# Kernel tuning notes

Hardware: AMD Instinct MI355X
Metric: run time of the kernel (lower is better)

## Reference

```python
import jax, jax.numpy as jnp
import numpy as np

N, E, D = 50000, 800000, 128   # nodes, edges, input feature dim
HEADS, HC = 8, 16
H = HEADS * HC                 # 128 hidden width after concat
G, OUT = 64, 16                # graphs in batch, output classes
EPS_BN = 1e-5


def _gat_conv(x, src, dst, edge_attr, W, att_src, att_dst, We, att_edge, b):
    """PyG GATConv (concat=True, negative_slope=0.2, add_self_loops=True,
    fill_value='mean' for edge_attr, dropout inactive in eval)."""
    n = x.shape[0]
    # self-loop edge attr = per-node mean of incoming edge attrs
    ones = jnp.ones((src.shape[0], 1), x.dtype)
    deg = jax.ops.segment_sum(ones, dst, num_segments=n)
    ea_mean = jax.ops.segment_sum(edge_attr, dst, num_segments=n) / jnp.maximum(deg, 1.0)
    loop = jnp.arange(n, dtype=src.dtype)
    src_f = jnp.concatenate([src, loop])
    dst_f = jnp.concatenate([dst, loop])
    ea = jnp.concatenate([edge_attr, ea_mean])          # [E+N, 1]
    h = (x @ W).reshape(n, HEADS, HC)                   # [N, heads, hc]
    a_src = jnp.sum(h * att_src, axis=-1)               # [N, heads]
    a_dst = jnp.sum(h * att_dst, axis=-1)               # [N, heads]
    he = (ea @ We).reshape(-1, HEADS, HC)               # [E+N, heads, hc]
    a_e = jnp.sum(he * att_edge, axis=-1)               # [E+N, heads]
    alpha = jax.nn.leaky_relu(a_src[src_f] + a_dst[dst_f] + a_e, 0.2)
    # segment softmax over destination nodes
    amax = jax.ops.segment_max(alpha, dst_f, num_segments=n)
    ex = jnp.exp(alpha - amax[dst_f])
    denom = jax.ops.segment_sum(ex, dst_f, num_segments=n)
    coef = ex / (denom[dst_f] + 1e-16)                  # [E+N, heads]
    out = jax.ops.segment_sum(h[src_f] * coef[..., None], dst_f, num_segments=n)
    return out.reshape(n, H) + b


def setup_inputs() -> dict:
    key = jax.random.key(0)
    k = lambda i: jax.random.fold_in(key, i)
    nrm = lambda i, shape, s=0.1: jax.random.normal(k(i), shape, dtype=jnp.float32) * s
    inp = {
        "x": jax.random.normal(k(0), (N, D), dtype=jnp.float32),
        "edge_index": jax.random.randint(k(1), (2, E), 0, N, dtype=jnp.int32),
        "edge_weights": jax.random.normal(k(2), (E, 1), dtype=jnp.float32),
        "batch": jnp.sort(jax.random.randint(k(3), (N,), 0, G, dtype=jnp.int32)),
        "bn_gamma": jnp.ones((D,), jnp.float32),
        "bn_beta": jnp.zeros((D,), jnp.float32),
        "bn_mean": nrm(4, (D,)),
        "bn_var": jax.random.uniform(k(5), (D,), dtype=jnp.float32) + 0.5,
    }
    ci = 10
    for li, ind in [(1, D), (2, H), (3, H)]:
        inp[f"W{li}"] = nrm(ci, (ind, H)); ci += 1
        inp[f"att_src{li}"] = nrm(ci, (HEADS, HC)); ci += 1
        inp[f"att_dst{li}"] = nrm(ci, (HEADS, HC)); ci += 1
        inp[f"We{li}"] = nrm(ci, (1, H)); ci += 1
        inp[f"att_edge{li}"] = nrm(ci, (HEADS, HC)); ci += 1
        inp[f"b{li}"] = jnp.zeros((H,), jnp.float32)
    inp["Wl1"] = nrm(40, (H, 2 * HC)); inp["bl1"] = jnp.zeros((2 * HC,), jnp.float32)
    inp["Wl2"] = nrm(41, (2 * HC, OUT)); inp["bl2"] = jnp.zeros((OUT,), jnp.float32)
    return inp


def reference(x, edge_index, edge_weights, batch,
              bn_gamma, bn_beta, bn_mean, bn_var,
              W1, att_src1, att_dst1, We1, att_edge1, b1,
              W2, att_src2, att_dst2, We2, att_edge2, b2,
              W3, att_src3, att_dst3, We3, att_edge3, b3,
              Wl1, bl1, Wl2, bl2):
    src, dst = edge_index[0], edge_index[1]
    # BatchNorm (eval mode, running stats)
    h = (x - bn_mean) / jnp.sqrt(bn_var + EPS_BN) * bn_gamma + bn_beta
    h = jax.nn.relu(_gat_conv(h, src, dst, edge_weights, W1, att_src1, att_dst1, We1, att_edge1, b1))
    h = jax.nn.relu(_gat_conv(h, src, dst, edge_weights, W2, att_src2, att_dst2, We2, att_edge2, b2))
    h = _gat_conv(h, src, dst, edge_weights, W3, att_src3, att_dst3, We3, att_edge3, b3)
    g = jax.ops.segment_max(h, batch, num_segments=G)   # global max pool -> [G, H]
    g = jax.nn.relu(g @ Wl1 + bl1)
    # dropout p=0.5 is identity in eval mode
    return g @ Wl2 + bl2
```

## Files before the change

kernel.cpp:

```cpp
#include <hip/hip_runtime.h>
#include <math.h>

#define NN 50000
#define NE 800000
#define NH 8
#define HDIM 128
#define NG 64
#define PSPLIT 16
#define MAXD 64

typedef __attribute__((ext_vector_type(8))) short bf16x8;
typedef __attribute__((ext_vector_type(4))) float f32x4;

static __device__ __forceinline__ float lrelu02(float x){ return x > 0.f ? x : 0.2f*x; }
static __device__ __forceinline__ unsigned short f2bf(float f){
    unsigned u = __float_as_uint(f);
    unsigned r = (u + 0x7FFFu + ((u >> 16) & 1u)) >> 16;
    return (unsigned short)r;
}
static __device__ __forceinline__ float bf2f(unsigned short h){ return __uint_as_float((unsigned)h << 16); }
static __device__ __forceinline__ float bf_lo(unsigned v){ return __uint_as_float(v << 16); }
static __device__ __forceinline__ float bf_hi(unsigned v){ return __uint_as_float(v & 0xFFFF0000u); }

__global__ void k_prep(const float* We1, const float* ae1, const float* We2, const float* ae2,
                       const float* We3, const float* ae3, float* wev,
                       const float* gam, const float* bet, const float* mean, const float* var,
                       float* sc, float* sh){
    int t = threadIdx.x;
    if (t < 128){
        float s = gam[t] * rsqrtf(var[t] + 1e-5f);
        sc[t] = s; sh[t] = bet[t] - mean[t] * s;
    } else if (t < 152){
        int q = t - 128; int l = q >> 3, hd = q & 7;
        const float* We = (l == 0) ? We1 : (l == 1) ? We2 : We3;
        const float* ae = (l == 0) ? ae1 : (l == 1) ? ae2 : ae3;
        float s = 0.f;
        for (int c = 0; c < 16; c++) s += We[hd*16+c] * ae[hd*16+c];
        wev[q] = s;
    }
}

__global__ void k_wprep(const float* W1, const float* W2, const float* W3,
                        unsigned short* Wth, unsigned short* Wtl){
    int i = blockIdx.x*256 + threadIdx.x;
    if (i >= 3*16384) return;
    int l = i >> 14, rem = i & 16383;
    int k = rem >> 7, n = rem & 127;
    const float* W = (l==0) ? W1 : (l==1) ? W2 : W3;
    float w = W[k*128 + n];
    unsigned short hi = f2bf(w);
    unsigned short lo = f2bf(w - bf2f(hi));
    Wth[l*16384 + n*128 + k] = hi;
    Wtl[l*16384 + n*128 + k] = lo;
}

__global__ void k_scatter(const int* srcp, const int* dstp, const float* ew,
                          unsigned long long* pk, unsigned* slab){
    int i = blockIdx.x*256 + threadIdx.x;
    if (i >= NE) return;
    int d = dstp[i];
    float w = ew[i];
    int fx = __float2int_rn(w * 16384.f);
    unsigned long long enc = ((unsigned long long)(unsigned)fx << 32) | 1ull;
    unsigned long long old = atomicAdd(&pk[d], enc);
    unsigned rank = (unsigned)(old & 0xFFFFFFFFull);
    if (rank < MAXD){
        unsigned ent = (unsigned)srcp[i] | ((unsigned)f2bf(w) << 16);
        __builtin_nontemporal_store(ent, &slab[(size_t)d*MAXD + rank]);
    }
}

__global__ __launch_bounds__(256, 3) void k_gemm(const float* A,
        const unsigned short* Wth, const unsigned short* Wtl,
        const float* sc, const float* sh,
        const float* att_s, const float* att_d,
        unsigned* Hb, float* a_src, float* a_dst, int M){
    __shared__ unsigned short Ah[64][132];
    __shared__ unsigned short Al[64][132];
    int t = threadIdx.x;
    int row0 = blockIdx.x * 64;
    int w = t >> 6, l = t & 63;
    int lr = l & 15, lg = l >> 4;

    {
        bool bn = (sc != nullptr);
        const float2* A2 = (const float2*)A;
        for (int i = 0; i < 16; i++){
            int idx2 = t + i*256;
            int r = idx2 >> 6, c2 = idx2 & 63;
            float2 v = make_float2(0.f, 0.f);
            if (row0 + r < M){
                v = A2[(size_t)(row0+r)*64 + c2];
                if (bn){
                    float2 s2 = ((const float2*)sc)[c2], h2 = ((const float2*)sh)[c2];
                    v.x = v.x*s2.x + h2.x; v.y = v.y*s2.y + h2.y;
                }
            }
            unsigned short h0 = f2bf(v.x), h1 = f2bf(v.y);
            unsigned short l0 = f2bf(v.x - bf2f(h0)), l1 = f2bf(v.y - bf2f(h1));
            ((unsigned*)&Ah[r][0])[c2] = (unsigned)h0 | ((unsigned)h1 << 16);
            ((unsigned*)&Al[r][0])[c2] = (unsigned)l0 | ((unsigned)l1 << 16);
        }
    }
    __syncthreads();

    f32x4 acc[4][2];
    #pragma unroll
    for (int m = 0; m < 4; m++){ acc[m][0] = (f32x4){0,0,0,0}; acc[m][1] = (f32x4){0,0,0,0}; }

    #pragma unroll
    for (int ks = 0; ks < 4; ks++){
        int kk = ks*32 + lg*8;
        bf16x8 bh0 = *(const bf16x8*)&Wth[((w*2+0)*16 + lr)*128 + kk];
        bf16x8 bl0 = *(const bf16x8*)&Wtl[((w*2+0)*16 + lr)*128 + kk];
        bf16x8 bh1 = *(const bf16x8*)&Wth[((w*2+1)*16 + lr)*128 + kk];
        bf16x8 bl1 = *(const bf16x8*)&Wtl[((w*2+1)*16 + lr)*128 + kk];
        #pragma unroll
        for (int m = 0; m < 4; m++){
            bf16x8 a_h = *(const bf16x8*)&Ah[m*16 + lr][kk];
            bf16x8 a_l = *(const bf16x8*)&Al[m*16 + lr][kk];
            acc[m][0] = __builtin_amdgcn_mfma_f32_16x16x32_bf16(a_h, bh0, acc[m][0], 0, 0, 0);
            acc[m][0] = __builtin_amdgcn_mfma_f32_16x16x32_bf16(a_h, bl0, acc[m][0], 0, 0, 0);
            acc[m][0] = __builtin_amdgcn_mfma_f32_16x16x32_bf16(a_l, bh0, acc[m][0], 0, 0, 0);
            acc[m][1] = __builtin_amdgcn_mfma_f32_16x16x32_bf16(a_h, bh1, acc[m][1], 0, 0, 0);
            acc[m][1] = __builtin_amdgcn_mfma_f32_16x16x32_bf16(a_h, bl1, acc[m][1], 0, 0, 0);
            acc[m][1] = __builtin_amdgcn_mfma_f32_16x16x32_bf16(a_l, bh1, acc[m][1], 0, 0, 0);
        }
    }

    float asv[2], adv[2];
    #pragma unroll
    for (int n = 0; n < 2; n++){
        asv[n] = att_s[(w*2+n)*16 + lr];
        adv[n] = att_d[(w*2+n)*16 + lr];
    }
    #pragma unroll
    for (int m = 0; m < 4; m++){
        #pragma unroll
        for (int n = 0; n < 2; n++){
            #pragma unroll
            for (int r = 0; r < 4; r++){
                float v = acc[m][n][r];
                float pv = __shfl_xor(v, 1);
                int row = row0 + m*16 + lg*4 + r;
                if (!(l & 1) && row < M){
                    unsigned d = (unsigned)f2bf(v) | ((unsigned)f2bf(pv) << 16);
                    Hb[(size_t)row*64 + w*16 + n*8 + (lr >> 1)] = d;
                }
            }
        }
    }
    #pragma unroll
    for (int m = 0; m < 4; m++){
        #pragma unroll
        for (int r = 0; r < 4; r++){
            int row = row0 + m*16 + lg*4 + r;
            #pragma unroll
            for (int n = 0; n < 2; n++){
                float ps = acc[m][n][r] * asv[n];
                float pd = acc[m][n][r] * adv[n];
                #pragma unroll
                for (int off = 1; off < 16; off <<= 1){
                    ps += __shfl_xor(ps, off);
                    pd += __shfl_xor(pd, off);
                }
                if (lr == 0 && row < M){
                    a_src[row*NH + w*2 + n] = ps;
                    a_dst[row*NH + w*2 + n] = pd;
                }
            }
        }
    }
}

__global__ __launch_bounds__(256) void k_aggr(const unsigned long long* pk, const unsigned* slab,
                       const float* a_src, const float* a_dst, const float* wev,
                       const unsigned* Hb, const float* bias, float* Out, int do_relu){
    int wid = threadIdx.x >> 6, lane = threadIdx.x & 63;
    int n = blockIdx.x*4 + wid;
    if (n >= NN) return;
    unsigned long long pv = pk[n];
    int dgt = (int)(unsigned)(pv & 0xFFFFFFFFull);
    int dg  = dgt < MAXD ? dgt : MAXD;
    float ea_self = (float)(int)(unsigned)(pv >> 32) * (1.f/16384.f) / fmaxf((float)dgt, 1.f);
    int hd = lane >> 3;
    float ad = a_dst[n*NH + hd];
    float wh = wev[hd];
    float accL0, accH0, den0, accL1 = 0.f, accH1 = 0.f, den1 = 0.f;
    {
        unsigned v = Hb[(size_t)n*64 + lane];
        float c = __expf(lrelu02(a_src[n*NH + hd] + ad + ea_self*wh));
        den0 = c; accL0 = c*bf_lo(v); accH0 = c*bf_hi(v);
    }
    const unsigned* srow = &slab[(size_t)n*MAXD];
    for (int base = 0; base < dg; base += 8){
        unsigned ent[8];
        #pragma unroll
        for (int j = 0; j < 8; j++){
            int ei = base + j;
            ent[j] = srow[ei < dg ? ei : dg - 1];
        }
        int src[8]; float eaw[8];
        #pragma unroll
        for (int j = 0; j < 8; j++){
            src[j] = (int)(ent[j] & 0xFFFFu);
            eaw[j] = bf2f((unsigned short)(ent[j] >> 16));
        }
        unsigned v[8];
        #pragma unroll
        for (int j = 0; j < 8; j++) v[j] = Hb[(size_t)src[j]*64 + lane];
        float as[8];
        #pragma unroll
        for (int j = 0; j < 8; j++) as[j] = a_src[src[j]*NH + hd];
        #pragma unroll
        for (int j = 0; j < 8; j++){
            float c = (base + j < dg) ? __expf(lrelu02(as[j] + ad + eaw[j]*wh)) : 0.f;
            if (j & 1){ den1 += c; accL1 += c*bf_lo(v[j]); accH1 += c*bf_hi(v[j]); }
            else      { den0 += c; accL0 += c*bf_lo(v[j]); accH0 += c*bf_hi(v[j]); }
        }
    }
    float inv = 1.f / (den0 + den1 + 1e-16f);
    float2 bv = ((const float2*)bias)[lane];
    float o0 = (accL0 + accL1) * inv + bv.x;
    float o1 = (accH0 + accH1) * inv + bv.y;
    if (do_relu){ o0 = fmaxf(o0, 0.f); o1 = fmaxf(o1, 0.f); }
    ((float2*)Out)[(size_t)n*64 + lane] = make_float2(o0, o1);
}

static __device__ int lower_bound_batch(const int* b, int v){
    int lo = 0, hi = NN;
    while (lo < hi){
        int mid = (lo + hi) >> 1;
        if (b[mid] < v) lo = mid + 1; else hi = mid;
    }
    return lo;
}

__global__ void k_pool1(const float* A, const int* batch, float* gpart){
    int g = blockIdx.x >> 4, s = blockIdx.x & (PSPLIT-1);
    int start = lower_bound_batch(batch, g);
    int end   = lower_bound_batch(batch, g + 1);
    int nrows = end - start;
    int chunk = (nrows + PSPLIT - 1) / PSPLIT;
    int rs = start + s*chunk;
    int re = rs + chunk; if (re > end) re = end;
    int col = threadIdx.x;
    float m = -INFINITY;
    for (int r = rs; r < re; r++) m = fmaxf(m, A[(size_t)r*HDIM + col]);
    gpart[(size_t)blockIdx.x*HDIM + col] = m;
}

__global__ void k_pool2(const float* gpart, float* gp){
    int g = blockIdx.x, col = threadIdx.x;
    float m = -INFINITY;
    for (int s = 0; s < PSPLIT; s++)
        m = fmaxf(m, gpart[(size_t)(g*PSPLIT+s)*HDIM + col]);
    gp[g*HDIM + col] = m;
}

__global__ __launch_bounds__(256) void k_mlp(const float* gp, const float* Wl1, const float* bl1,
                      const float* Wl2, const float* bl2, float* out){
    __shared__ float gl[NG*HDIM];
    __shared__ float t1[NG*32];
    int t = threadIdx.x;
    for (int i = 0; i < 8; i++)
        ((float4*)gl)[t + i*256] = ((const float4*)gp)[t + i*256];
    __syncthreads();
    for (int i = 0; i < 8; i++){
        int o = t + i*256;
        int gi = o >> 5, j = o & 31;
        float s = bl1[j];
        for (int k = 0; k < 128; k++) s += gl[gi*128 + k] * Wl1[k*32 + j];
        t1[o] = fmaxf(s, 0.f);
    }
    __syncthreads();
    for (int i = 0; i < 4; i++){
        int o = t + i*256;
        int gi = o >> 4, j = o & 15;
        float s = bl2[j];
        for (int k = 0; k < 32; k++) s += t1[gi*32 + k] * Wl2[k*16 + j];
        out[o] = s;
    }
}

extern "C" void kernel_launch(void* const* d_in, const int* in_sizes, int n_in,
                              void* d_out, int out_size, void* d_ws, size_t ws_size,
                              hipStream_t stream){
    const float* x    = (const float*)d_in[0];
    const int*   ei   = (const int*)d_in[1];
    const float* ew   = (const float*)d_in[2];
    const int*   batch= (const int*)d_in[3];
    const float* bng  = (const float*)d_in[4];
    const float* bnb  = (const float*)d_in[5];
    const float* bnm  = (const float*)d_in[6];
    const float* bnv  = (const float*)d_in[7];
    const float* Wmat[3] = {(const float*)d_in[8],  (const float*)d_in[14], (const float*)d_in[20]};
    const float* asr[3]  = {(const float*)d_in[9],  (const float*)d_in[15], (const float*)d_in[21]};
    const float* adt[3]  = {(const float*)d_in[10], (const float*)d_in[16], (const float*)d_in[22]};
    const float* Wep[3]  = {(const float*)d_in[11], (const float*)d_in[17], (const float*)d_in[23]};
    const float* aep[3]  = {(const float*)d_in[12], (const float*)d_in[18], (const float*)d_in[24]};
    const float* bp[3]   = {(const float*)d_in[13], (const float*)d_in[19], (const float*)d_in[25]};
    const float* Wl1 = (const float*)d_in[26];
    const float* bl1 = (const float*)d_in[27];
    const float* Wl2 = (const float*)d_in[28];
    const float* bl2 = (const float*)d_in[29];

    char* p = (char*)d_ws;
    auto alloc = [&](size_t bytes)->char*{
        char* r = p; p += (bytes + 255) & ~(size_t)255; return r;
    };
    float*    bufA  = (float*)alloc((size_t)NN*HDIM*4);
    unsigned* Hb    = (unsigned*)alloc((size_t)NN*64*4);
    float*    a_src = (float*)alloc((size_t)NN*NH*4);
    float*    a_dst = (float*)alloc((size_t)NN*NH*4);
    unsigned long long* pk = (unsigned long long*)alloc((size_t)NN*8);
    unsigned* slab  = (unsigned*)alloc((size_t)NN*MAXD*4);
    float*    wev   = (float*)alloc(24*4);
    float*    scv   = (float*)alloc(128*4);
    float*    shv   = (float*)alloc(128*4);
    unsigned short* Wth = (unsigned short*)alloc((size_t)3*16384*2);
    unsigned short* Wtl = (unsigned short*)alloc((size_t)3*16384*2);
    float*    gpart = (float*)alloc((size_t)NG*PSPLIT*HDIM*4);
    float*    gpool = (float*)alloc((size_t)NG*HDIM*4);

    const int* srcp = ei;
    const int* dstp = ei + NE;

    hipMemsetAsync(pk, 0, (size_t)NN*8, stream);
    k_prep<<<1, 256, 0, stream>>>(Wep[0], aep[0], Wep[1], aep[1], Wep[2], aep[2], wev,
                                  bng, bnb, bnm, bnv, scv, shv);
    k_wprep<<<192, 256, 0, stream>>>(Wmat[0], Wmat[1], Wmat[2], Wth, Wtl);
    k_scatter<<<(NE+255)/256, 256, 0, stream>>>(srcp, dstp, ew, pk, slab);

    for (int l = 0; l < 3; l++){
        const float* A  = (l == 0) ? x : bufA;
        const float* sc = (l == 0) ? scv : nullptr;
        const float* sh = (l == 0) ? shv : nullptr;
        k_gemm<<<(NN+63)/64, 256, 0, stream>>>(A, Wth + l*16384, Wtl + l*16384, sc, sh,
                                               asr[l], adt[l], Hb, a_src, a_dst, NN);
        k_aggr<<<(NN+3)/4, 256, 0, stream>>>(pk, slab, a_src, a_dst, wev + l*8,
                                             Hb, bp[l], bufA, (l < 2) ? 1 : 0);
    }
    k_pool1<<<NG*PSPLIT, 128, 0, stream>>>(bufA, batch, gpart);
    k_pool2<<<NG, 128, 0, stream>>>(gpart, gpool);
    k_mlp<<<1, 256, 0, stream>>>(gpool, Wl1, bl1, Wl2, bl2, (float*)d_out);
}
```

Measured before the change: 324.1 us.

## Split aggregation wave into two half-waves per edge and vectorize edge scatter

The aggregation kernel now has each half-wave (32 lanes, 4 features per lane via uint2 loads) handle alternate edges of a node, combining the partial sums with a cross-half shuffle. It also switches to a grid-stride persistent launch of 2048 blocks. This doubles the edges in flight per wave and widens the per-lane gathers to cut latency-bound gather time. The scatter kernel processes four edges per thread with vector loads and issues its atomics back to back, which assumes NE is divisible by 4.

```diff
diff --git a/kernel.cpp b/kernel.cpp
--- a/kernel.cpp
+++ b/kernel.cpp
@@ -56,17 +56,28 @@
 
 __global__ void k_scatter(const int* srcp, const int* dstp, const float* ew,
                           unsigned long long* pk, unsigned* slab){
-    int i = blockIdx.x*256 + threadIdx.x;
-    if (i >= NE) return;
-    int d = dstp[i];
-    float w = ew[i];
-    int fx = __float2int_rn(w * 16384.f);
-    unsigned long long enc = ((unsigned long long)(unsigned)fx << 32) | 1ull;
-    unsigned long long old = atomicAdd(&pk[d], enc);
-    unsigned rank = (unsigned)(old & 0xFFFFFFFFull);
-    if (rank < MAXD){
-        unsigned ent = (unsigned)srcp[i] | ((unsigned)f2bf(w) << 16);
-        __builtin_nontemporal_store(ent, &slab[(size_t)d*MAXD + rank]);
+    int i0 = (blockIdx.x*256 + threadIdx.x)*4;
+    if (i0 >= NE) return;
+    int4   d4 = *(const int4*)&dstp[i0];
+    float4 w4 = *(const float4*)&ew[i0];
+    int4   s4 = *(const int4*)&srcp[i0];
+    int   d[4] = {d4.x, d4.y, d4.z, d4.w};
+    float w[4] = {w4.x, w4.y, w4.z, w4.w};
+    int   s[4] = {s4.x, s4.y, s4.z, s4.w};
+    unsigned long long old[4];
+    #pragma unroll
+    for (int j = 0; j < 4; j++){
+        int fx = __float2int_rn(w[j] * 16384.f);
+        unsigned long long enc = ((unsigned long long)(unsigned)fx << 32) | 1ull;
+        old[j] = atomicAdd(&pk[d[j]], enc);
+    }
+    #pragma unroll
+    for (int j = 0; j < 4; j++){
+        unsigned rank = (unsigned)(old[j] & 0xFFFFFFFFull);
+        if (rank < MAXD){
+            unsigned ent = (unsigned)s[j] | ((unsigned)f2bf(w[j]) << 16);
+            __builtin_nontemporal_store(ent, &slab[(size_t)d[j]*MAXD + rank]);
+        }
     }
 }
 
@@ -177,54 +188,69 @@
                        const float* a_src, const float* a_dst, const float* wev,
                        const unsigned* Hb, const float* bias, float* Out, int do_relu){
     int wid = threadIdx.x >> 6, lane = threadIdx.x & 63;
-    int n = blockIdx.x*4 + wid;
-    if (n >= NN) return;
-    unsigned long long pv = pk[n];
-    int dgt = (int)(unsigned)(pv & 0xFFFFFFFFull);
-    int dg  = dgt < MAXD ? dgt : MAXD;
-    float ea_self = (float)(int)(unsigned)(pv >> 32) * (1.f/16384.f) / fmaxf((float)dgt, 1.f);
-    int hd = lane >> 3;
-    float ad = a_dst[n*NH + hd];
-    float wh = wev[hd];
-    float accL0, accH0, den0, accL1 = 0.f, accH1 = 0.f, den1 = 0.f;
-    {
-        unsigned v = Hb[(size_t)n*64 + lane];
-        float c = __expf(lrelu02(a_src[n*NH + hd] + ad + ea_self*wh));
-        den0 = c; accL0 = c*bf_lo(v); accH0 = c*bf_hi(v);
-    }
-    const unsigned* srow = &slab[(size_t)n*MAXD];
-    for (int base = 0; base < dg; base += 8){
-        unsigned ent[8];
-        #pragma unroll
-        for (int j = 0; j < 8; j++){
-            int ei = base + j;
-            ent[j] = srow[ei < dg ? ei : dg - 1];
-        }
-        int src[8]; float eaw[8];
-        #pragma unroll
-        for (int j = 0; j < 8; j++){
-            src[j] = (int)(ent[j] & 0xFFFFu);
-            eaw[j] = bf2f((unsigned short)(ent[j] >> 16));
-        }
-        unsigned v[8];
-        #pragma unroll
-        for (int j = 0; j < 8; j++) v[j] = Hb[(size_t)src[j]*64 + lane];
-        float as[8];
-        #pragma unroll
-        for (int j = 0; j < 8; j++) as[j] = a_src[src[j]*NH + hd];
-        #pragma unroll
-        for (int j = 0; j < 8; j++){
-            float c = (base + j < dg) ? __expf(lrelu02(as[j] + ad + eaw[j]*wh)) : 0.f;
-            if (j & 1){ den1 += c; accL1 += c*bf_lo(v[j]); accH1 += c*bf_hi(v[j]); }
-            else      { den0 += c; accL0 += c*bf_lo(v[j]); accH0 += c*bf_hi(v[j]); }
-        }
-    }
-    float inv = 1.f / (den0 + den1 + 1e-16f);
-    float2 bv = ((const float2*)bias)[lane];
-    float o0 = (accL0 + accL1) * inv + bv.x;
-    float o1 = (accH0 + accH1) * inv + bv.y;
-    if (do_relu){ o0 = fmaxf(o0, 0.f); o1 = fmaxf(o1, 0.f); }
-    ((float2*)Out)[(size_t)n*64 + lane] = make_float2(o0, o1);
+    int gw = blockIdx.x*4 + wid;
+    int q = lane & 31, h = lane >> 5;
+    int head = q >> 2;
+    float wh = wev[head];
+    float4 bv = ((const float4*)bias)[q];
+    for (int n = gw; n < NN; n += 8192){
+        unsigned long long pv = pk[n];
+        int dgt = (int)(unsigned)(pv & 0xFFFFFFFFull);
+        int dg  = dgt < MAXD ? dgt : MAXD;
+        float ea_self = (float)(int)(unsigned)(pv >> 32) * (1.f/16384.f) / fmaxf((float)dgt, 1.f);
+        float ad = a_dst[n*NH + head];
+        float a0=0.f, a1=0.f, a2=0.f, a3=0.f, den=0.f;
+        {
+            uint2 v = *(const uint2*)&Hb[(size_t)n*64 + q*2];
+            float c = __expf(lrelu02(a_src[n*NH + head] + ad + ea_self*wh));
+            if (h) c = 0.f;
+            den += c;
+            a0 += c*bf_lo(v.x); a1 += c*bf_hi(v.x);
+            a2 += c*bf_lo(v.y); a3 += c*bf_hi(v.y);
+        }
+        const unsigned* srow = &slab[(size_t)n*MAXD];
+        for (int base = 0; base < dg; base += 16){
+            unsigned ent[8]; int ei[8];
+            #pragma unroll
+            for (int j = 0; j < 8; j++){
+                ei[j] = base + j*2 + h;
+                ent[j] = srow[ei[j] < dg ? ei[j] : 0];
+            }
+            int src[8]; float eaw[8];
+            #pragma unroll
+            for (int j = 0; j < 8; j++){
+                src[j] = (int)(ent[j] & 0xFFFFu);
+                eaw[j] = bf2f((unsigned short)(ent[j] >> 16));
+            }
+            uint2 v[8];
+            #pragma unroll
+            for (int j = 0; j < 8; j++) v[j] = *(const uint2*)&Hb[(size_t)src[j]*64 + q*2];
+            float as[8];
+            #pragma unroll
+            for (int j = 0; j < 8; j++) as[j] = a_src[src[j]*NH + head];
+            #pragma unroll
+            for (int j = 0; j < 8; j++){
+                float c = (ei[j] < dg) ? __expf(lrelu02(as[j] + ad + eaw[j]*wh)) : 0.f;
+                den += c;
+                a0 += c*bf_lo(v[j].x); a1 += c*bf_hi(v[j].x);
+                a2 += c*bf_lo(v[j].y); a3 += c*bf_hi(v[j].y);
+            }
+        }
+        a0 += __shfl_xor(a0, 32); a1 += __shfl_xor(a1, 32);
+        a2 += __shfl_xor(a2, 32); a3 += __shfl_xor(a3, 32);
+        den += __shfl_xor(den, 32);
+        float inv = 1.f / (den + 1e-16f);
+        if (lane < 32){
+            float4 o;
+            o.x = a0*inv + bv.x; o.y = a1*inv + bv.y;
+            o.z = a2*inv + bv.z; o.w = a3*inv + bv.w;
+            if (do_relu){
+                o.x = fmaxf(o.x, 0.f); o.y = fmaxf(o.y, 0.f);
+                o.z = fmaxf(o.z, 0.f); o.w = fmaxf(o.w, 0.f);
+            }
+            ((float4*)Out)[(size_t)n*32 + q] = o;
+        }
+    }
 }
 
 static __device__ int lower_bound_batch(const int* b, int v){
@@ -330,7 +356,7 @@
     k_prep<<<1, 256, 0, stream>>>(Wep[0], aep[0], Wep[1], aep[1], Wep[2], aep[2], wev,
                                   bng, bnb, bnm, bnv, scv, shv);
     k_wprep<<<192, 256, 0, stream>>>(Wmat[0], Wmat[1], Wmat[2], Wth, Wtl);
-    k_scatter<<<(NE+255)/256, 256, 0, stream>>>(srcp, dstp, ew, pk, slab);
+    k_scatter<<<(NE/4+255)/256, 256, 0, stream>>>(srcp, dstp, ew, pk, slab);
 
     for (int l = 0; l < 3; l++){
         const float* A  = (l == 0) ? x : bufA;
@@ -338,8 +364,8 @@
         const float* sh = (l == 0) ? shv : nullptr;
         k_gemm<<<(NN+63)/64, 256, 0, stream>>>(A, Wth + l*16384, Wtl + l*16384, sc, sh,
                                                asr[l], adt[l], Hb, a_src, a_dst, NN);
-        k_aggr<<<(NN+3)/4, 256, 0, stream>>>(pk, slab, a_src, a_dst, wev + l*8,
-                                             Hb, bp[l], bufA, (l < 2) ? 1 : 0);
+        k_aggr<<<2048, 256, 0, stream>>>(pk, slab, a_src, a_dst, wev + l*8,
+                                         Hb, bp[l], bufA, (l < 2) ? 1 : 0);
     }
     k_pool1<<<NG*PSPLIT, 128, 0, stream>>>(bufA, batch, gpart);
     k_pool2<<<NG, 128, 0, stream>>>(gpart, gpool);
```

New measurement: 346.2 us. +6.8%, slower.
